# Kernel optimization log

Hardware: AMD Instinct MI355X
Metric: run time of the kernel (lower is better)

## Reference

```python
import jax, jax.numpy as jnp
import numpy as np

B, O, Q, QD, SG = 8, 1024, 2048, 1024, 1200

def setup_inputs() -> dict:
    key = jax.random.key(0)
    k1, k2, k3 = jax.random.split(key, 3)
    query_in = jax.random.normal(k1, (B, O, QD), dtype=jnp.float32)
    context_in = jax.random.normal(k2, (B, Q, SG), dtype=jnp.float32)
    # linear_in.weight initialized uniform(-0.1, 0.1) in the torch module
    W = jax.random.uniform(k3, (SG, QD), dtype=jnp.float32, minval=-0.1, maxval=0.1)
    return {"query_in": query_in, "context_in": context_in, "W": W}

def reference(query_in, context_in, W):
    # general attention: project query from query_dim -> sg_dim (no bias)
    query = jnp.einsum('boq,sq->bos', query_in, W)          # [B, O, SG]
    scores = jnp.einsum('bos,bqs->boq', query, context_in)   # [B, O, Q] (unscaled)
    weights = jax.nn.softmax(scores, axis=-1)                # [B, O, Q]
    mix = jnp.einsum('boq,bqs->bos', weights, context_in)    # [B, O, SG]
    return (mix, weights)
```

## Files before the change

### kernel.cpp

```cpp
#include <hip/hip_runtime.h>
#include <hip/hip_bf16.h>


typedef _Float16 half8 __attribute__((ext_vector_type(8)));
typedef _Float16 half4v __attribute__((ext_vector_type(4)));
typedef float    f32x4 __attribute__((ext_vector_type(4)));

#define AS1C(p) ((const __attribute__((address_space(1))) void*)(p))
#define AS3(p)  ((__attribute__((address_space(3))) void*)(p))

__device__ __forceinline__ void stage_tile(const _Float16* __restrict__ X, _Float16* s,
                                           int t, long row0, long rowmax, int ld, int k0)
{
#pragma unroll
    for (int j = 0; j < 2; ++j) {
        const int L = t + 256 * j;
        const int r = L >> 2;
        const int slot = L & 3;
        const int koff = slot ^ ((r >> 1) & 3);
        long grow = row0 + r; if (grow > rowmax) grow = rowmax;
        const _Float16* src = X + grow * (long)ld + k0 + koff * 8;
        _Float16* dst = s + (long)((t & ~63) + 256 * j) * 8;
        __builtin_amdgcn_global_load_lds(AS1C(src), AS3(dst), 16, 0, 0);
    }
}

__device__ __forceinline__ half8 frag(const _Float16* s, int row, int kslot)
{
    return *(const half8*)(s + row * 32 + ((kslot ^ ((row >> 1) & 3)) << 3));
}

template<bool SPLIT, bool OUT16>
__global__ __launch_bounds__(256) void gemm16(
    const _Float16* __restrict__ Ah, const _Float16* __restrict__ Al,
    const _Float16* __restrict__ Bh, const _Float16* __restrict__ Bl,
    float* __restrict__ Cf, _Float16* __restrict__ Ch, _Float16* __restrict__ Cl,
    int N, int K, int lda, int ldb, int ldc,
    long sA, long sB, long sC)
{
    const int t = threadIdx.x;
    const int bz = blockIdx.z;
    const _Float16* A_h = Ah + bz * sA;
    const _Float16* B_h = Bh + bz * sB;
    const _Float16* A_l = SPLIT ? (Al + bz * sA) : nullptr;
    const _Float16* B_l = SPLIT ? (Bl + bz * sB) : nullptr;

    __shared__ __align__(16) _Float16 sAh[128 * 32];
    __shared__ __align__(16) _Float16 sBh[128 * 32];
    __shared__ __align__(16) _Float16 sAl[SPLIT ? 128 * 32 : 8];
    __shared__ __align__(16) _Float16 sBl[SPLIT ? 128 * 32 : 8];

    const long row0 = (long)blockIdx.y * 128;
    const int  col0 = blockIdx.x * 128;

    const int wid = t >> 6, lane = t & 63;
    const int wm = (wid >> 1) * 64, wn = (wid & 1) * 64;
    const int fr = lane & 15, kslot = lane >> 4;

    f32x4 acc[4][4];
#pragma unroll
    for (int i = 0; i < 4; ++i)
#pragma unroll
        for (int j = 0; j < 4; ++j) acc[i][j] = (f32x4){0.f, 0.f, 0.f, 0.f};

    for (int k0 = 0; k0 < K; k0 += 32) {
        __syncthreads();
        stage_tile(A_h, sAh, t, row0, row0 + 127, lda, k0);
        stage_tile(B_h, sBh, t, col0, N - 1, ldb, k0);
        if (SPLIT) {
            stage_tile(A_l, sAl, t, row0, row0 + 127, lda, k0);
            stage_tile(B_l, sBl, t, col0, N - 1, ldb, k0);
        }
        __syncthreads();

        half8 a_h[4], b_h[4], a_l[4], b_l[4];
#pragma unroll
        for (int i = 0; i < 4; ++i) {
            a_h[i] = frag(sAh, wm + i * 16 + fr, kslot);
            b_h[i] = frag(sBh, wn + i * 16 + fr, kslot);
            if (SPLIT) {
                a_l[i] = frag(sAl, wm + i * 16 + fr, kslot);
                b_l[i] = frag(sBl, wn + i * 16 + fr, kslot);
            }
        }
#pragma unroll
        for (int mi = 0; mi < 4; ++mi)
#pragma unroll
            for (int ni = 0; ni < 4; ++ni) {
                acc[mi][ni] = __builtin_amdgcn_mfma_f32_16x16x32_f16(a_h[mi], b_h[ni], acc[mi][ni], 0, 0, 0);
                if (SPLIT) {
                    acc[mi][ni] = __builtin_amdgcn_mfma_f32_16x16x32_f16(a_h[mi], b_l[ni], acc[mi][ni], 0, 0, 0);
                    acc[mi][ni] = __builtin_amdgcn_mfma_f32_16x16x32_f16(a_l[mi], b_h[ni], acc[mi][ni], 0, 0, 0);
                }
            }
    }

    const int r4 = (lane >> 4) * 4;
    float* C_f = OUT16 ? nullptr : (Cf + bz * sC);
#pragma unroll
    for (int mi = 0; mi < 4; ++mi)
#pragma unroll
        for (int ni = 0; ni < 4; ++ni) {
            const int colg = col0 + wn + ni * 16 + fr;
#pragma unroll
            for (int r = 0; r < 4; ++r) {
                const long rowg = row0 + wm + mi * 16 + r4 + r;
                const float v = acc[mi][ni][r];
                if (OUT16) {
                    if (colg < ldc) {
                        const float vv = (colg < N) ? v : 0.f;
                        const _Float16 hi = (_Float16)vv;
                        const _Float16 lo = (_Float16)(vv - (float)hi);
                        Ch[rowg * ldc + colg] = hi;
                        Cl[rowg * ldc + colg] = lo;
                    }
                } else {
                    if (colg < N) C_f[rowg * (long)ldc + colg] = v;
                }
            }
        }
}

__global__ __launch_bounds__(256) void cvt_split(const float* __restrict__ X,
    _Float16* __restrict__ H, _Float16* __restrict__ L,
    long total4, int cin4, int cout4)
{
    for (long i = (long)blockIdx.x * 256 + threadIdx.x; i < total4; i += (long)gridDim.x * 256) {
        const long r = i / cout4;
        const int  c = (int)(i - r * cout4);
        float4 v = make_float4(0.f, 0.f, 0.f, 0.f);
        if (c < cin4) v = *(const float4*)(X + (r * cin4 + c) * 4);
        const _Float16 h0 = (_Float16)v.x, h1 = (_Float16)v.y, h2 = (_Float16)v.z, h3 = (_Float16)v.w;
        const _Float16 l0 = (_Float16)(v.x - (float)h0), l1 = (_Float16)(v.y - (float)h1);
        const _Float16 l2 = (_Float16)(v.z - (float)h2), l3 = (_Float16)(v.w - (float)h3);
        *(half4v*)(H + (r * cout4 + c) * 4) = (half4v){h0, h1, h2, h3};
        *(half4v*)(L + (r * cout4 + c) * 4) = (half4v){l0, l1, l2, l3};
    }
}

__global__ __launch_bounds__(256) void tcvt(const float* __restrict__ X, _Float16* __restrict__ Y)
{
    const int b = blockIdx.z;
    const float* Xb = X + (long)b * 2048 * 1200;
    _Float16* Yb = Y + (long)b * 1200 * 2048;
    __shared__ _Float16 tl[32][33];
    const int tx = threadIdx.x & 31, ty = threadIdx.x >> 5;
    const int s0 = blockIdx.x * 32, q0 = blockIdx.y * 32;
#pragma unroll
    for (int p = 0; p < 4; ++p) {
        const int q = q0 + ty + p * 8, s = s0 + tx;
        const float v = (s < 1200) ? Xb[(long)q * 1200 + s] : 0.f;
        tl[tx][ty + p * 8] = (_Float16)v;
    }
    __syncthreads();
#pragma unroll
    for (int p = 0; p < 4; ++p) {
        const int s = s0 + ty + p * 8;
        if (s < 1200) Yb[(long)s * 2048 + q0 + tx] = tl[ty + p * 8][tx];
    }
}

__global__ __launch_bounds__(256) void softmax_k(float* __restrict__ w, _Float16* __restrict__ w16)
{
    float* p = w + (long)blockIdx.x * 2048;
    half4v* p16 = (half4v*)(w16 + (long)blockIdx.x * 2048);
    const int t = threadIdx.x;
    float4 v0 = ((const float4*)p)[t];
    float4 v1 = ((const float4*)p)[t + 256];

    float m = fmaxf(fmaxf(fmaxf(v0.x, v0.y), fmaxf(v0.z, v0.w)),
                    fmaxf(fmaxf(v1.x, v1.y), fmaxf(v1.z, v1.w)));
#pragma unroll
    for (int off = 1; off < 64; off <<= 1) m = fmaxf(m, __shfl_xor(m, off));
    __shared__ float redm[4], reds[4];
    const int wave = t >> 6, lane = t & 63;
    if (lane == 0) redm[wave] = m;
    __syncthreads();
    m = fmaxf(fmaxf(redm[0], redm[1]), fmaxf(redm[2], redm[3]));

    float e[8];
    e[0] = __expf(v0.x - m); e[1] = __expf(v0.y - m);
    e[2] = __expf(v0.z - m); e[3] = __expf(v0.w - m);
    e[4] = __expf(v1.x - m); e[5] = __expf(v1.y - m);
    e[6] = __expf(v1.z - m); e[7] = __expf(v1.w - m);

    float s = ((e[0] + e[1]) + (e[2] + e[3])) + ((e[4] + e[5]) + (e[6] + e[7]));
#pragma unroll
    for (int off = 1; off < 64; off <<= 1) s += __shfl_xor(s, off);
    if (lane == 0) reds[wave] = s;
    __syncthreads();
    s = (reds[0] + reds[1]) + (reds[2] + reds[3]);

    const float inv = 1.0f / s;
    float o0 = e[0] * inv, o1 = e[1] * inv, o2 = e[2] * inv, o3 = e[3] * inv;
    float o4 = e[4] * inv, o5 = e[5] * inv, o6 = e[6] * inv, o7 = e[7] * inv;
    ((float4*)p)[t]       = make_float4(o0, o1, o2, o3);
    ((float4*)p)[t + 256] = make_float4(o4, o5, o6, o7);
    p16[t]       = (half4v){(_Float16)o0, (_Float16)o1, (_Float16)o2, (_Float16)o3};
    p16[t + 256] = (half4v){(_Float16)o4, (_Float16)o5, (_Float16)o6, (_Float16)o7};
}

extern "C" void kernel_launch(void* const* d_in, const int* in_sizes, int n_in,
                              void* d_out, int out_size, void* d_ws, size_t ws_size,
                              hipStream_t stream)
{
    const float* query_in = (const float*)d_in[0];
    const float* context  = (const float*)d_in[1];
    const float* W        = (const float*)d_in[2];

    float* mix    = (float*)d_out;
    float* scores = (float*)d_out + 9830400LL;

    _Float16* qh  = (_Float16*)d_ws;
    _Float16* ql  = qh  + 8388608;
    _Float16* wh  = ql  + 8388608;
    _Float16* wl  = wh  + 1228800;
    _Float16* ch  = wl  + 1228800;
    _Float16* cl  = ch  + 19922944;
    _Float16* ct  = cl  + 19922944;
    _Float16* qeh = ct  + 19660800;
    _Float16* qel = qeh + 9961472;
    _Float16* w16 = qel + 9961472;

    dim3 blk(256);

    cvt_split<<<2048, blk, 0, stream>>>(query_in, qh, ql, 8192L * 256, 256, 256);
    cvt_split<<<512,  blk, 0, stream>>>(W,        wh, wl, 1200L * 256, 256, 256);
    cvt_split<<<2048, blk, 0, stream>>>(context,  ch, cl, 16384L * 304, 300, 304);
    tcvt<<<dim3(38, 64, 8), blk, 0, stream>>>(context, ct);

    gemm16<true, true><<<dim3(10, 64, 1), blk, 0, stream>>>(
        qh, ql, wh, wl, nullptr, qeh, qel,
        1200, 1024, 1024, 1024, 1216, 0, 0, 0);

    gemm16<true, false><<<dim3(16, 8, 8), blk, 0, stream>>>(
        qeh, qel, ch, cl, scores, nullptr, nullptr,
        2048, 1216, 1216, 1216, 2048, 1024L * 1216, 2048L * 1216, 1024L * 2048);

    softmax_k<<<dim3(8192), blk, 0, stream>>>(scores, w16);

    gemm16<false, false><<<dim3(10, 8, 8), blk, 0, stream>>>(
        w16, nullptr, ct, nullptr, mix, nullptr, nullptr,
        1200, 2048, 2048, 2048, 1200, 1024L * 2048, 1200L * 2048, 1024L * 1200);
}
```

Measured before the change: 574.2 us.

## Double-buffer GEMM LDS tiles and fuse fp16 conversion kernels

The GEMM now stages two LDS buffers and prefetches the next K tile with global_load_lds while running MFMAs on the current one, leaving one barrier per iteration. The query and W split conversions merge into one kernel, and the context hi/lo split is fused with the transpose so context is read once. This aims to hide global load latency and cut launch and memory traffic. Doubling LDS usage may reduce occupancy for the split GEMMs.

```diff
diff --git a/kernel.cpp b/kernel.cpp
--- a/kernel.cpp
+++ b/kernel.cpp
@@ -45,10 +45,10 @@
     const _Float16* A_l = SPLIT ? (Al + bz * sA) : nullptr;
     const _Float16* B_l = SPLIT ? (Bl + bz * sB) : nullptr;
 
-    __shared__ __align__(16) _Float16 sAh[128 * 32];
-    __shared__ __align__(16) _Float16 sBh[128 * 32];
-    __shared__ __align__(16) _Float16 sAl[SPLIT ? 128 * 32 : 8];
-    __shared__ __align__(16) _Float16 sBl[SPLIT ? 128 * 32 : 8];
+    __shared__ __align__(16) _Float16 sAh[2][128 * 32];
+    __shared__ __align__(16) _Float16 sBh[2][128 * 32];
+    __shared__ __align__(16) _Float16 sAl[SPLIT ? 2 : 1][SPLIT ? 128 * 32 : 8];
+    __shared__ __align__(16) _Float16 sBl[SPLIT ? 2 : 1][SPLIT ? 128 * 32 : 8];
 
     const long row0 = (long)blockIdx.y * 128;
     const int  col0 = blockIdx.x * 128;
@@ -63,24 +63,34 @@
 #pragma unroll
         for (int j = 0; j < 4; ++j) acc[i][j] = (f32x4){0.f, 0.f, 0.f, 0.f};
 
+    stage_tile(A_h, sAh[0], t, row0, row0 + 127, lda, 0);
+    stage_tile(B_h, sBh[0], t, col0, N - 1, ldb, 0);
+    if (SPLIT) {
+        stage_tile(A_l, sAl[0], t, row0, row0 + 127, lda, 0);
+        stage_tile(B_l, sBl[0], t, col0, N - 1, ldb, 0);
+    }
+    __syncthreads();
+
+    int cur = 0;
     for (int k0 = 0; k0 < K; k0 += 32) {
-        __syncthreads();
-        stage_tile(A_h, sAh, t, row0, row0 + 127, lda, k0);
-        stage_tile(B_h, sBh, t, col0, N - 1, ldb, k0);
-        if (SPLIT) {
-            stage_tile(A_l, sAl, t, row0, row0 + 127, lda, k0);
-            stage_tile(B_l, sBl, t, col0, N - 1, ldb, k0);
+        if (k0 + 32 < K) {
+            const int nxt = cur ^ 1, kn = k0 + 32;
+            stage_tile(A_h, sAh[nxt], t, row0, row0 + 127, lda, kn);
+            stage_tile(B_h, sBh[nxt], t, col0, N - 1, ldb, kn);
+            if (SPLIT) {
+                stage_tile(A_l, sAl[nxt], t, row0, row0 + 127, lda, kn);
+                stage_tile(B_l, sBl[nxt], t, col0, N - 1, ldb, kn);
+            }
         }
-        __syncthreads();
 
         half8 a_h[4], b_h[4], a_l[4], b_l[4];
 #pragma unroll
         for (int i = 0; i < 4; ++i) {
-            a_h[i] = frag(sAh, wm + i * 16 + fr, kslot);
-            b_h[i] = frag(sBh, wn + i * 16 + fr, kslot);
+            a_h[i] = frag(sAh[cur], wm + i * 16 + fr, kslot);
+            b_h[i] = frag(sBh[cur], wn + i * 16 + fr, kslot);
             if (SPLIT) {
-                a_l[i] = frag(sAl, wm + i * 16 + fr, kslot);
-                b_l[i] = frag(sBl, wn + i * 16 + fr, kslot);
+                a_l[i] = frag(sAl[cur], wm + i * 16 + fr, kslot);
+                b_l[i] = frag(sBl[cur], wn + i * 16 + fr, kslot);
             }
         }
 #pragma unroll
@@ -93,6 +103,9 @@
                     acc[mi][ni] = __builtin_amdgcn_mfma_f32_16x16x32_f16(a_l[mi], b_h[ni], acc[mi][ni], 0, 0, 0);
                 }
             }
+
+        __syncthreads();
+        cur ^= 1;
     }
 
     const int r4 = (lane >> 4) * 4;
@@ -121,28 +134,33 @@
         }
 }
 
-__global__ __launch_bounds__(256) void cvt_split(const float* __restrict__ X,
-    _Float16* __restrict__ H, _Float16* __restrict__ L,
-    long total4, int cin4, int cout4)
-{
-    for (long i = (long)blockIdx.x * 256 + threadIdx.x; i < total4; i += (long)gridDim.x * 256) {
-        const long r = i / cout4;
-        const int  c = (int)(i - r * cout4);
-        float4 v = make_float4(0.f, 0.f, 0.f, 0.f);
-        if (c < cin4) v = *(const float4*)(X + (r * cin4 + c) * 4);
+__global__ __launch_bounds__(256) void qw_cvt(
+    const float* __restrict__ Q, _Float16* __restrict__ QH, _Float16* __restrict__ QL,
+    const float* __restrict__ Wt, _Float16* __restrict__ WH, _Float16* __restrict__ WL)
+{
+    const long NQ = 8192L * 1024 / 4;
+    const long NT = NQ + 1200L * 1024 / 4;
+    for (long i = (long)blockIdx.x * 256 + threadIdx.x; i < NT; i += (long)gridDim.x * 256) {
+        const float* src; _Float16 *dh, *dl; long j;
+        if (i < NQ) { j = i; src = Q; dh = QH; dl = QL; }
+        else        { j = i - NQ; src = Wt; dh = WH; dl = WL; }
+        float4 v = *(const float4*)(src + j * 4);
         const _Float16 h0 = (_Float16)v.x, h1 = (_Float16)v.y, h2 = (_Float16)v.z, h3 = (_Float16)v.w;
         const _Float16 l0 = (_Float16)(v.x - (float)h0), l1 = (_Float16)(v.y - (float)h1);
         const _Float16 l2 = (_Float16)(v.z - (float)h2), l3 = (_Float16)(v.w - (float)h3);
-        *(half4v*)(H + (r * cout4 + c) * 4) = (half4v){h0, h1, h2, h3};
-        *(half4v*)(L + (r * cout4 + c) * 4) = (half4v){l0, l1, l2, l3};
-    }
-}
-
-__global__ __launch_bounds__(256) void tcvt(const float* __restrict__ X, _Float16* __restrict__ Y)
+        *(half4v*)(dh + j * 4) = (half4v){h0, h1, h2, h3};
+        *(half4v*)(dl + j * 4) = (half4v){l0, l1, l2, l3};
+    }
+}
+
+__global__ __launch_bounds__(256) void ctx_prep(const float* __restrict__ X,
+    _Float16* __restrict__ H, _Float16* __restrict__ L, _Float16* __restrict__ T)
 {
     const int b = blockIdx.z;
     const float* Xb = X + (long)b * 2048 * 1200;
-    _Float16* Yb = Y + (long)b * 1200 * 2048;
+    _Float16* Hb = H + (long)b * 2048 * 1216;
+    _Float16* Lb = L + (long)b * 2048 * 1216;
+    _Float16* Tb = T + (long)b * 1200 * 2048;
     __shared__ _Float16 tl[32][33];
     const int tx = threadIdx.x & 31, ty = threadIdx.x >> 5;
     const int s0 = blockIdx.x * 32, q0 = blockIdx.y * 32;
@@ -150,13 +168,16 @@
     for (int p = 0; p < 4; ++p) {
         const int q = q0 + ty + p * 8, s = s0 + tx;
         const float v = (s < 1200) ? Xb[(long)q * 1200 + s] : 0.f;
-        tl[tx][ty + p * 8] = (_Float16)v;
+        const _Float16 hi = (_Float16)v;
+        Hb[(long)q * 1216 + s] = hi;
+        Lb[(long)q * 1216 + s] = (_Float16)(v - (float)hi);
+        tl[tx][ty + p * 8] = hi;
     }
     __syncthreads();
 #pragma unroll
     for (int p = 0; p < 4; ++p) {
         const int s = s0 + ty + p * 8;
-        if (s < 1200) Yb[(long)s * 2048 + q0 + tx] = tl[ty + p * 8][tx];
+        if (s < 1200) Tb[(long)s * 2048 + q0 + tx] = tl[ty + p * 8][tx];
     }
 }
 
@@ -224,10 +245,8 @@
 
     dim3 blk(256);
 
-    cvt_split<<<2048, blk, 0, stream>>>(query_in, qh, ql, 8192L * 256, 256, 256);
-    cvt_split<<<512,  blk, 0, stream>>>(W,        wh, wl, 1200L * 256, 256, 256);
-    cvt_split<<<2048, blk, 0, stream>>>(context,  ch, cl, 16384L * 304, 300, 304);
-    tcvt<<<dim3(38, 64, 8), blk, 0, stream>>>(context, ct);
+    qw_cvt<<<2400, blk, 0, stream>>>(query_in, qh, ql, W, wh, wl);
+    ctx_prep<<<dim3(38, 64, 8), blk, 0, stream>>>(context, ch, cl, ct);
 
     gemm16<true, true><<<dim3(10, 64, 1), blk, 0, stream>>>(
         qh, ql, wh, wl, nullptr, qeh, qel,
```

After: 532.8 us. 7.2% less time.
